# Kernel optimization log

Hardware: AMD Instinct MI355X
Metric: run time of the kernel (lower is better)

## Reference

```python
import jax, jax.numpy as jnp
import numpy as np

# OGB/PyG molecular featurization vocab sizes (x_map / e_map)
NODE_VOCABS = [119, 9, 11, 12, 10, 5, 8, 2, 2]   # 9 atom features
EDGE_VOCABS = [22, 6, 2]                          # 3 bond features
HID, OUT, LAYERS = 128, 256, 3
N_NODES, N_EDGES, N_GRAPHS = 200000, 400000, 8000
NODE_OFF = np.concatenate([[0], np.cumsum(NODE_VOCABS)[:-1]]).astype(np.int32)
EDGE_OFF = np.concatenate([[0], np.cumsum(EDGE_VOCABS)[:-1]]).astype(np.int32)
NODE_TOT = int(np.sum(NODE_VOCABS))
EDGE_TOT = int(np.sum(EDGE_VOCABS))


def setup_inputs() -> dict:
    key = jax.random.key(0)
    ks = jax.random.split(key, 16)
    # integer graph data (values in-range per categorical column via modulo)
    x = jax.random.randint(ks[0], (N_NODES, 9), 0, 1 << 30) % jnp.asarray(NODE_VOCABS)
    edge_attr = jax.random.randint(ks[1], (N_EDGES, 3), 0, 1 << 30) % jnp.asarray(EDGE_VOCABS)
    edge_index = jax.random.randint(ks[2], (2, N_EDGES), 0, N_NODES)
    batch = jnp.sort(jax.random.randint(ks[3], (N_NODES,), 0, N_GRAPHS))
    s = 0.02
    return {
        "x": x, "edge_attr": edge_attr, "edge_index": edge_index, "batch": batch,
        # embedding tables packed row-wise with per-feature offsets
        "node_emb": jax.random.normal(ks[4], (NODE_TOT, HID), jnp.float32) * s,
        "edge_emb": jax.random.normal(ks[5], (EDGE_TOT, HID), jnp.float32) * s,
        "node_proj_w": jax.random.normal(ks[6], (9 * HID, HID), jnp.float32) * s,
        "node_proj_b": jnp.zeros((HID,), jnp.float32),
        "edge_proj_w": jax.random.normal(ks[7], (3 * HID, HID), jnp.float32) * s,
        "edge_proj_b": jnp.zeros((HID,), jnp.float32),
        "mlp_w1": jax.random.normal(ks[8], (LAYERS, HID, HID), jnp.float32) * s,
        "mlp_b1": jnp.zeros((LAYERS, HID), jnp.float32),
        "mlp_w2": jax.random.normal(ks[9], (LAYERS, HID, HID), jnp.float32) * s,
        "mlp_b2": jnp.zeros((LAYERS, HID), jnp.float32),
        "proj_w": jax.random.normal(ks[10], (HID, OUT), jnp.float32) * s,
        "proj_b": jnp.zeros((OUT,), jnp.float32),
    }


def reference(x, edge_attr, edge_index, batch,
              node_emb, edge_emb,
              node_proj_w, node_proj_b, edge_proj_w, edge_proj_b,
              mlp_w1, mlp_b1, mlp_w2, mlp_b2, proj_w, proj_b):
    n = x.shape[0]
    e = edge_attr.shape[0]
    # embedding lookup per categorical column, concat, project -> [N, HID]
    nf = node_emb[x + jnp.asarray(NODE_OFF)].reshape(n, 9 * HID)
    h = nf @ node_proj_w + node_proj_b
    ef = edge_emb[edge_attr + jnp.asarray(EDGE_OFF)].reshape(e, 3 * HID)
    ef = ef @ edge_proj_w + edge_proj_b
    src, dst = edge_index[0], edge_index[1]
    for l in range(LAYERS):
        # GINEConv (eps=0): mlp(x + sum_{j->i} relu(x_j + e_ji)), then outer relu
        m = jax.nn.relu(h[src] + ef)                       # [E, HID] gather + fuse
        agg = jax.ops.segment_sum(m, dst, num_segments=N_NODES)
        z = h + agg
        z = jax.nn.relu(z @ mlp_w1[l] + mlp_b1[l]) @ mlp_w2[l] + mlp_b2[l]
        h = jax.nn.relu(z)
    g = jax.ops.segment_sum(h, batch, num_segments=N_GRAPHS)  # global_add_pool
    p = g @ proj_w + proj_b
    norm = jnp.maximum(jnp.linalg.norm(p, axis=-1, keepdims=True), 1e-12)
    return p / norm
```

## Files before the change

kernel.cpp:

```cpp
#include <hip/hip_runtime.h>
#include <hip/hip_bf16.h>

#define NN 200000
#define NE 400000
#define NG 8000
#define HID 128
#define OUTD 256
#define NODE_TOT 178
#define EDGE_TOT 30
#define NCOMBO 264
#define SCAN_NB 196

typedef __attribute__((ext_vector_type(8))) short bfrag8;
typedef __attribute__((ext_vector_type(4))) short bfrag4;
typedef __attribute__((ext_vector_type(4))) float f32x4;
typedef unsigned short ushort_t;

__constant__ int c_noff[10] = {0,119,128,139,151,161,166,174,176,178};

__device__ __forceinline__ ushort_t f2bf(float f) {
  union { float f; unsigned u; } x; x.f = f;
  unsigned r = x.u + 0x7fffu + ((x.u >> 16) & 1u);
  return (ushort_t)(r >> 16);
}
__device__ __forceinline__ float bf2f(ushort_t u) {
  union { unsigned u; float f; } x; x.u = ((unsigned)u) << 16;
  return x.f;
}

__global__ __launch_bounds__(128) void build_tables(
    const float* __restrict__ node_emb, const float* __restrict__ edge_emb,
    const float* __restrict__ npw, const float* __restrict__ npb,
    const float* __restrict__ epw, const float* __restrict__ epb,
    float* __restrict__ PN, float* __restrict__ PE)
{
  int r = blockIdx.x, d = threadIdx.x;
  if (r < NODE_TOT) {
    int c = 0;
    while (r >= c_noff[c+1]) c++;
    float acc = (c == 0) ? npb[d] : 0.f;
    const float* er = node_emb + r*HID;
    const float* wb = npw + (size_t)(c*HID)*HID + d;
    for (int k = 0; k < HID; k++) acc += er[k] * wb[(size_t)k*HID];
    PN[r*HID + d] = acc;
  } else {
    int re = r - NODE_TOT;
    int c = (re >= 28) ? 2 : (re >= 22 ? 1 : 0);
    float acc = (c == 0) ? epb[d] : 0.f;
    const float* er = edge_emb + re*HID;
    const float* wb = epw + (size_t)(c*HID)*HID + d;
    for (int k = 0; k < HID; k++) acc += er[k] * wb[(size_t)k*HID];
    PE[re*HID + d] = acc;
  }
}

__global__ __launch_bounds__(64) void build_pe3(const float* __restrict__ PE,
                                                unsigned* __restrict__ pe3b)
{
  int c = blockIdx.x, lane = threadIdx.x;
  int a2 = c & 1, a1 = (c >> 1) % 6, a0 = (c >> 1) / 6;
  int d = lane*2;
  float v0 = PE[a0*HID + d]   + PE[(22+a1)*HID + d]   + PE[(28+a2)*HID + d];
  float v1 = PE[a0*HID + d+1] + PE[(22+a1)*HID + d+1] + PE[(28+a2)*HID + d+1];
  pe3b[c*64 + lane] = (unsigned)f2bf(v0) | ((unsigned)f2bf(v1) << 16);
}

__global__ __launch_bounds__(256) void pack_w1(const float* __restrict__ w1,
                                               ushort_t* __restrict__ pw)
{
  int t = blockIdx.x*256 + threadIdx.x;
  int lane = t & 63, tile = (t >> 6) & 31, layer = t >> 11;
  int nt = tile >> 2, kt = tile & 3;
  int n  = nt*16 + (lane & 15);
  int k0 = kt*32 + ((lane >> 4) << 3);
  const float* src = w1 + (size_t)layer*HID*HID;
  ushort_t* dst = pw + (size_t)layer*32768 + (size_t)tile*512 + lane*8;
  #pragma unroll
  for (int j = 0; j < 8; j++) dst[j] = f2bf(src[(size_t)(k0+j)*HID + n]);
}

__global__ __launch_bounds__(256) void pack_w2(const float* __restrict__ w2,
                                               ushort_t* __restrict__ pw)
{
  int t = blockIdx.x*256 + threadIdx.x;
  int lane = t & 63, frag = (t >> 6) & 63, layer = t >> 12;
  int it = frag >> 3, kk = frag & 7;
  int i  = it*16 + (lane & 15);
  int k0 = kk*16 + ((lane >> 4) << 2);
  const float* src = w2 + (size_t)layer*HID*HID;
  ushort_t* dst = pw + (size_t)layer*32768 + 16384 + (size_t)frag*256 + lane*4;
  #pragma unroll
  for (int j = 0; j < 4; j++) dst[j] = f2bf(src[(size_t)(k0+j)*HID + i]);
}

__global__ __launch_bounds__(256) void node_embed(const int* __restrict__ x,
                                                  const float* __restrict__ PN,
                                                  ushort_t* __restrict__ h)
{
  int gid = blockIdx.x*256 + threadIdx.x;
  int i = gid >> 5, d0 = (gid & 31) << 2;
  const int* xr = x + i*9;
  f32x4 acc = {0.f, 0.f, 0.f, 0.f};
  #pragma unroll
  for (int c = 0; c < 9; c++)
    acc += *(const f32x4*)&PN[(c_noff[c] + xr[c])*HID + d0];
  uint2 pk;
  pk.x = (unsigned)f2bf(acc[0]) | ((unsigned)f2bf(acc[1]) << 16);
  pk.y = (unsigned)f2bf(acc[2]) | ((unsigned)f2bf(acc[3]) << 16);
  *(uint2*)&h[(size_t)i*HID + d0] = pk;
}

__global__ __launch_bounds__(256) void hist(const int* __restrict__ ei, int* __restrict__ deg) {
  int e = blockIdx.x*256 + threadIdx.x;
  if (e < NE) atomicAdd(&deg[ei[NE + e]], 1);
}

__global__ __launch_bounds__(256) void scan1(const int* __restrict__ deg,
                                             int* __restrict__ rowptr,
                                             int* __restrict__ bsum)
{
  __shared__ int sd[256];
  int b = blockIdx.x, t = threadIdx.x;
  int idx0 = b*1024 + t*4;
  int v[4]; int s = 0;
  #pragma unroll
  for (int j = 0; j < 4; j++) { int i = idx0 + j; v[j] = (i < NN) ? deg[i] : 0; s += v[j]; }
  sd[t] = s; __syncthreads();
  for (int off = 1; off < 256; off <<= 1) {
    int x = (t >= off) ? sd[t - off] : 0; __syncthreads();
    sd[t] += x; __syncthreads();
  }
  int run = (t > 0) ? sd[t-1] : 0;
  #pragma unroll
  for (int j = 0; j < 4; j++) { int i = idx0 + j; run += v[j]; if (i < NN) rowptr[i+1] = run; }
  if (t == 255) bsum[b] = sd[255];
}

__global__ __launch_bounds__(256) void scan2(int* __restrict__ bsum) {
  __shared__ int sd[256];
  int t = threadIdx.x;
  sd[t] = (t < SCAN_NB) ? bsum[t] : 0; __syncthreads();
  for (int off = 1; off < 256; off <<= 1) {
    int x = (t >= off) ? sd[t - off] : 0; __syncthreads();
    sd[t] += x; __syncthreads();
  }
  if (t < SCAN_NB) bsum[t] = sd[t];
}

__global__ __launch_bounds__(256) void scan3(int* __restrict__ rowptr, const int* __restrict__ bsum) {
  int b = blockIdx.x, t = threadIdx.x;
  if (b == 0) { if (t == 0) rowptr[0] = 0; return; }
  int add = bsum[b-1];
  int idx0 = b*1024 + t*4;
  #pragma unroll
  for (int j = 0; j < 4; j++) { int i = idx0 + j; if (i < NN) rowptr[i+1] += add; }
}

__global__ __launch_bounds__(256) void scatter_e(const int* __restrict__ ei,
                                                 const int* __restrict__ ea,
                                                 int* __restrict__ cursor,
                                                 unsigned* __restrict__ elist,
                                                 unsigned char* __restrict__ dloc)
{
  int e = blockIdx.x*256 + threadIdx.x;
  if (e >= NE) return;
  int src = ei[e], dst = ei[NE + e];
  const int* ar = ea + e*3;
  unsigned combo = (unsigned)((ar[0]*6 + ar[1])*2 + ar[2]);
  int pos = atomicAdd(&cursor[dst], 1);
  elist[pos] = (unsigned)src | (combo << 18);
  dloc[pos] = (unsigned char)(dst & 63);
}

template<bool LAST>
__global__ __launch_bounds__(256, 4) void gine_layer(
    const ushort_t* __restrict__ hin, ushort_t* __restrict__ hout,
    const int* __restrict__ rowptr, const unsigned* __restrict__ elist,
    const unsigned char* __restrict__ dloc,
    const unsigned* __restrict__ pe3b,
    const ushort_t* __restrict__ pw,
    const float* __restrict__ b1, const float* __restrict__ b2,
    const int* __restrict__ batch, float* __restrict__ gf)
{
  __shared__ ushort_t aggs[64*136];
  __shared__ int bids[64];
  int tid = threadIdx.x;
  int w = tid >> 6, lane = tid & 63;
  int q = lane >> 4;
  int rb = blockIdx.x*64 + w*16;
  const unsigned* h2 = (const unsigned*)hin;

  if (LAST && tid < 64) bids[tid] = batch[blockIdx.x*64 + tid];

  #pragma unroll
  for (int r = 0; r < 16; r++)
    ((unsigned*)&aggs[(w*16 + r)*136])[lane] = 0;

  int s = rowptr[rb], E = rowptr[rb + 16];
  int cur = -1;
  float ax = 0.f, ay = 0.f;

  auto proc = [&](int dl, unsigned hv, unsigned tt) {
    int dlu = __builtin_amdgcn_readfirstlane(dl);
    if (dlu != cur) {
      if (cur >= 0)
        ((unsigned*)&aggs[cur*136])[lane] =
            (unsigned)f2bf(ax) | ((unsigned)f2bf(ay) << 16);
      cur = dlu; ax = 0.f; ay = 0.f;
    }
    ax += fmaxf(bf2f((ushort_t)(hv & 0xffff)) + bf2f((ushort_t)(tt & 0xffff)), 0.f);
    ay += fmaxf(bf2f((ushort_t)(hv >> 16)) + bf2f((ushort_t)(tt >> 16)), 0.f);
  };

  int j = s;
  for (; j + 7 < E; j += 8) {
    unsigned pk[8]; int dl[8]; unsigned hv[8], tt[8];
    #pragma unroll
    for (int k = 0; k < 8; k++) { pk[k] = elist[j+k]; dl[k] = dloc[j+k]; }
    #pragma unroll
    for (int k = 0; k < 8; k++) {
      hv[k] = h2[(size_t)(pk[k] & 0x3ffff)*64 + lane];
      tt[k] = pe3b[(pk[k] >> 18)*64 + lane];
    }
    #pragma unroll
    for (int k = 0; k < 8; k++) proc(dl[k], hv[k], tt[k]);
  }
  for (; j < E; ++j) {
    unsigned pk = elist[j];
    int dl = dloc[j];
    unsigned hv = h2[(size_t)(pk & 0x3ffff)*64 + lane];
    unsigned tt = pe3b[(pk >> 18)*64 + lane];
    proc(dl, hv, tt);
  }
  if (cur >= 0)
    ((unsigned*)&aggs[cur*136])[lane] =
        (unsigned)f2bf(ax) | ((unsigned)f2bf(ay) << 16);

  int n = rb + (lane & 15);
  int acol = q << 3;

  bfrag8 afr[4];
  #pragma unroll
  for (int kt = 0; kt < 4; kt++) {
    int c = kt*32 + acol;
    bfrag8 hfr = *(const bfrag8*)(hin + (size_t)n*HID + c);
    bfrag8 gfr = *(const bfrag8*)&aggs[(w*16 + (lane & 15))*136 + c];
    bfrag8 fr;
    #pragma unroll
    for (int j2 = 0; j2 < 8; j2++)
      fr[j2] = (short)f2bf(bf2f((ushort_t)hfr[j2]) + bf2f((ushort_t)gfr[j2]));
    afr[kt] = fr;
  }

  if (LAST) __syncthreads();

  const bfrag8* w1f = (const bfrag8*)pw;
  const bfrag4* w2f = (const bfrag4*)(pw + 16384);

  f32x4 acc1[8];
  #pragma unroll
  for (int nt = 0; nt < 8; nt++)
    acc1[nt] = *(const f32x4*)&b1[nt*16 + q*4];
  #pragma unroll
  for (int kt = 0; kt < 4; kt++)
    #pragma unroll
    for (int nt = 0; nt < 8; nt++)
      acc1[nt] = __builtin_amdgcn_mfma_f32_16x16x32_bf16(w1f[(nt*4+kt)*64 + lane], afr[kt], acc1[nt], 0, 0, 0);

  bfrag4 t4[8];
  #pragma unroll
  for (int kk = 0; kk < 8; kk++) {
    bfrag4 v;
    #pragma unroll
    for (int r = 0; r < 4; r++) v[r] = (short)f2bf(fmaxf(acc1[kk][r], 0.f));
    t4[kk] = v;
  }

  #pragma unroll
  for (int it = 0; it < 8; it++) {
    f32x4 acc2 = *(const f32x4*)&b2[it*16 + q*4];
    #pragma unroll
    for (int kk = 0; kk < 8; kk++)
      acc2 = __builtin_amdgcn_mfma_f32_16x16x16bf16_1k(w2f[(it*8+kk)*64 + lane], t4[kk], acc2, 0, 0, 0);
    uint2 pk;
    pk.x = (unsigned)f2bf(fmaxf(acc2[0], 0.f)) | ((unsigned)f2bf(fmaxf(acc2[1], 0.f)) << 16);
    pk.y = (unsigned)f2bf(fmaxf(acc2[2], 0.f)) | ((unsigned)f2bf(fmaxf(acc2[3], 0.f)) << 16);
    if (LAST) {
      *(uint2*)&aggs[(w*16 + (lane & 15))*136 + it*16 + q*4] = pk;
    } else {
      *(uint2*)&hout[(size_t)n*HID + it*16 + q*4] = pk;
    }
  }

  if (LAST) {
    __syncthreads();
    int d = tid & 127, rh = tid >> 7;
    float acc = 0.f;
    int curg = bids[rh*32];
    for (int r = 0; r < 32; r++) {
      int row = rh*32 + r;
      int g = bids[row];
      if (g != curg) {
        atomicAdd(&gf[(size_t)curg*HID + d], acc);
        acc = 0.f; curg = g;
      }
      acc += bf2f(aggs[row*136 + d]);
    }
    atomicAdd(&gf[(size_t)curg*HID + d], acc);
  }
}

__global__ __launch_bounds__(256) void final_proj(const float* __restrict__ gf,
                                                  const float* __restrict__ W,
                                                  const float* __restrict__ b,
                                                  float* __restrict__ out)
{
  __shared__ float gls[16*128];
  __shared__ float part[16][4];
  int tid = threadIdx.x;
  int gbase = blockIdx.x*16;
  for (int idx = tid; idx < 2048; idx += 256) gls[idx] = gf[(size_t)gbase*128 + idx];
  __syncthreads();
  float acc[16];
  #pragma unroll
  for (int g = 0; g < 16; g++) acc[g] = 0.f;
  for (int k = 0; k < 128; k++) {
    float wv = W[(size_t)k*256 + tid];
    #pragma unroll
    for (int g = 0; g < 16; g++) acc[g] += gls[g*128 + k] * wv;
  }
  float bj = b[tid];
  int wid = tid >> 6, lane = tid & 63;
  #pragma unroll
  for (int g = 0; g < 16; g++) {
    acc[g] += bj;
    float s = acc[g]*acc[g];
    #pragma unroll
    for (int off = 32; off > 0; off >>= 1) s += __shfl_xor(s, off, 64);
    if (lane == 0) part[g][wid] = s;
  }
  __syncthreads();
  #pragma unroll
  for (int g = 0; g < 16; g++) {
    float S = part[g][0] + part[g][1] + part[g][2] + part[g][3];
    float rn = 1.f / fmaxf(sqrtf(S), 1e-12f);
    out[(size_t)(gbase + g)*256 + tid] = acc[g]*rn;
  }
}

__global__ __launch_bounds__(256) void ws_diag(float* __restrict__ out, int n, float wsval) {
  int i = blockIdx.x*256 + threadIdx.x;
  if (i < n) out[i] = (i == 0) ? wsval : 0.f;
}

extern "C" void kernel_launch(void* const* d_in, const int* in_sizes, int n_in,
                              void* d_out, int out_size, void* d_ws, size_t ws_size,
                              hipStream_t stream)
{
  const int*   x     = (const int*)d_in[0];
  const int*   ea    = (const int*)d_in[1];
  const int*   ei    = (const int*)d_in[2];
  const int*   batch = (const int*)d_in[3];
  const float* nemb  = (const float*)d_in[4];
  const float* eemb  = (const float*)d_in[5];
  const float* npw   = (const float*)d_in[6];
  const float* npb   = (const float*)d_in[7];
  const float* epw   = (const float*)d_in[8];
  const float* epb   = (const float*)d_in[9];
  const float* w1    = (const float*)d_in[10];
  const float* b1    = (const float*)d_in[11];
  const float* w2    = (const float*)d_in[12];
  const float* b2    = (const float*)d_in[13];
  const float* pjw   = (const float*)d_in[14];
  const float* pjb   = (const float*)d_in[15];
  float* out = (float*)d_out;

  char* ws = (char*)d_ws;
  size_t off = 0;
  auto carve = [&](size_t bytes) -> char* {
    char* p = ws + off;
    off = (off + bytes + 255) & ~(size_t)255;
    return p;
  };
  float*    PN     = (float*)carve((size_t)NODE_TOT*HID*4);
  float*    PE     = (float*)carve((size_t)EDGE_TOT*HID*4);
  unsigned* PE3b   = (unsigned*)carve((size_t)NCOMBO*64*4);
  ushort_t* PW     = (ushort_t*)carve((size_t)3*32768*2);
  ushort_t* hA     = (ushort_t*)carve((size_t)NN*HID*2);
  ushort_t* hB     = (ushort_t*)carve((size_t)NN*HID*2);
  float*    gf     = (float*)carve((size_t)NG*HID*4);
  int*      deg    = (int*)carve((size_t)NN*4);
  int*      rowptr = (int*)carve((size_t)(NN+1)*4);
  int*      cursor = (int*)carve((size_t)NN*4);
  int*      bsum   = (int*)carve((size_t)SCAN_NB*4);
  unsigned* elist  = (unsigned*)carve((size_t)NE*4);
  unsigned char* dlc = (unsigned char*)carve((size_t)NE);

  if (off > ws_size) {
    ws_diag<<<(out_size + 255)/256, 256, 0, stream>>>(out, out_size, (float)ws_size);
    return;
  }

  build_tables<<<NODE_TOT + EDGE_TOT, 128, 0, stream>>>(nemb, eemb, npw, npb, epw, epb, PN, PE);
  build_pe3<<<NCOMBO, 64, 0, stream>>>(PE, PE3b);
  pack_w1<<<24, 256, 0, stream>>>(w1, PW);
  pack_w2<<<48, 256, 0, stream>>>(w2, PW);
  node_embed<<<(NN*32)/256, 256, 0, stream>>>(x, PN, hA);

  hipMemsetAsync(deg, 0, (size_t)NN*4, stream);
  hipMemsetAsync(gf, 0, (size_t)NG*HID*4, stream);
  hist<<<(NE + 255)/256, 256, 0, stream>>>(ei, deg);
  scan1<<<SCAN_NB, 256, 0, stream>>>(deg, rowptr, bsum);
  scan2<<<1, 256, 0, stream>>>(bsum);
  scan3<<<SCAN_NB, 256, 0, stream>>>(rowptr, bsum);
  hipMemcpyAsync(cursor, rowptr, (size_t)NN*4, hipMemcpyDeviceToDevice, stream);
  scatter_e<<<(NE + 255)/256, 256, 0, stream>>>(ei, ea, cursor, elist, dlc);

  gine_layer<false><<<NN/64, 256, 0, stream>>>(hA, hB, rowptr, elist, dlc, PE3b,
                                               PW, b1, b2, batch, gf);
  gine_layer<false><<<NN/64, 256, 0, stream>>>(hB, hA, rowptr, elist, dlc, PE3b,
                                               PW + 32768, b1 + HID, b2 + HID, batch, gf);
  gine_layer<true><<<NN/64, 256, 0, stream>>>(hA, hB, rowptr, elist, dlc, PE3b,
                                              PW + 65536, b1 + 2*HID, b2 + 2*HID, batch, gf);

  final_proj<<<NG/16, 256, 0, stream>>>(gf, pjw, pjb, out);
}
```

Baseline: 447.9 us.

## Balance edge aggregation across warps with LDS float atomics and fuse setup launches

The edge aggregation in each GINE layer used to give every wavefront its own 16 destination rows, which left work unbalanced when degrees differed. It now splits the block's whole edge range evenly across the four wavefronts, and they accumulate into a shared fp32 LDS buffer with atomicAdd. Keeping the aggregate in fp32 also drops the bf16 rounding before the MLP. On the setup side, the two weight-pack kernels are merged, the scan writes the cursor copy directly so the memcpy goes away, and the two memsets become one. The cost is LDS atomic traffic, two atomics per element per edge, plus a larger shared-memory footprint that may lower occupancy.

```diff
diff --git a/kernel.cpp b/kernel.cpp
--- a/kernel.cpp
+++ b/kernel.cpp
@@ -10,6 +10,7 @@
 #define EDGE_TOT 30
 #define NCOMBO 264
 #define SCAN_NB 196
+#define AST 132
 
 typedef __attribute__((ext_vector_type(8))) short bfrag8;
 typedef __attribute__((ext_vector_type(4))) short bfrag4;
@@ -65,32 +66,31 @@
   pe3b[c*64 + lane] = (unsigned)f2bf(v0) | ((unsigned)f2bf(v1) << 16);
 }
 
-__global__ __launch_bounds__(256) void pack_w1(const float* __restrict__ w1,
-                                               ushort_t* __restrict__ pw)
+__global__ __launch_bounds__(256) void pack_w(const float* __restrict__ w1,
+                                              const float* __restrict__ w2,
+                                              ushort_t* __restrict__ pw)
 {
   int t = blockIdx.x*256 + threadIdx.x;
-  int lane = t & 63, tile = (t >> 6) & 31, layer = t >> 11;
-  int nt = tile >> 2, kt = tile & 3;
-  int n  = nt*16 + (lane & 15);
-  int k0 = kt*32 + ((lane >> 4) << 3);
-  const float* src = w1 + (size_t)layer*HID*HID;
-  ushort_t* dst = pw + (size_t)layer*32768 + (size_t)tile*512 + lane*8;
-  #pragma unroll
-  for (int j = 0; j < 8; j++) dst[j] = f2bf(src[(size_t)(k0+j)*HID + n]);
-}
-
-__global__ __launch_bounds__(256) void pack_w2(const float* __restrict__ w2,
-                                               ushort_t* __restrict__ pw)
-{
-  int t = blockIdx.x*256 + threadIdx.x;
-  int lane = t & 63, frag = (t >> 6) & 63, layer = t >> 12;
-  int it = frag >> 3, kk = frag & 7;
-  int i  = it*16 + (lane & 15);
-  int k0 = kk*16 + ((lane >> 4) << 2);
-  const float* src = w2 + (size_t)layer*HID*HID;
-  ushort_t* dst = pw + (size_t)layer*32768 + 16384 + (size_t)frag*256 + lane*4;
-  #pragma unroll
-  for (int j = 0; j < 4; j++) dst[j] = f2bf(src[(size_t)(k0+j)*HID + i]);
+  if (t < 6144) {
+    int lane = t & 63, tile = (t >> 6) & 31, layer = t >> 11;
+    int nt = tile >> 2, kt = tile & 3;
+    int n  = nt*16 + (lane & 15);
+    int k0 = kt*32 + ((lane >> 4) << 3);
+    const float* src = w1 + (size_t)layer*HID*HID;
+    ushort_t* dst = pw + (size_t)layer*32768 + (size_t)tile*512 + lane*8;
+    #pragma unroll
+    for (int j = 0; j < 8; j++) dst[j] = f2bf(src[(size_t)(k0+j)*HID + n]);
+  } else {
+    int t2 = t - 6144;
+    int lane = t2 & 63, frag = (t2 >> 6) & 63, layer = t2 >> 12;
+    int it = frag >> 3, kk = frag & 7;
+    int i  = it*16 + (lane & 15);
+    int k0 = kk*16 + ((lane >> 4) << 2);
+    const float* src = w2 + (size_t)layer*HID*HID;
+    ushort_t* dst = pw + (size_t)layer*32768 + 16384 + (size_t)frag*256 + lane*4;
+    #pragma unroll
+    for (int j = 0; j < 4; j++) dst[j] = f2bf(src[(size_t)(k0+j)*HID + i]);
+  }
 }
 
 __global__ __launch_bounds__(256) void node_embed(const int* __restrict__ x,
@@ -147,13 +147,23 @@
   if (t < SCAN_NB) bsum[t] = sd[t];
 }
 
-__global__ __launch_bounds__(256) void scan3(int* __restrict__ rowptr, const int* __restrict__ bsum) {
+__global__ __launch_bounds__(256) void scan3(int* __restrict__ rowptr,
+                                             const int* __restrict__ bsum,
+                                             int* __restrict__ cursor)
+{
   int b = blockIdx.x, t = threadIdx.x;
-  if (b == 0) { if (t == 0) rowptr[0] = 0; return; }
-  int add = bsum[b-1];
+  int add = (b > 0) ? bsum[b-1] : 0;
+  if (b == 0 && t == 0) { rowptr[0] = 0; cursor[0] = 0; }
   int idx0 = b*1024 + t*4;
   #pragma unroll
-  for (int j = 0; j < 4; j++) { int i = idx0 + j; if (i < NN) rowptr[i+1] += add; }
+  for (int j = 0; j < 4; j++) {
+    int i = idx0 + j;
+    if (i < NN) {
+      int v = rowptr[i+1] + add;
+      rowptr[i+1] = v;
+      cursor[i+1] = v;
+    }
+  }
 }
 
 __global__ __launch_bounds__(256) void scatter_e(const int* __restrict__ ei,
@@ -182,38 +192,27 @@
     const float* __restrict__ b1, const float* __restrict__ b2,
     const int* __restrict__ batch, float* __restrict__ gf)
 {
-  __shared__ ushort_t aggs[64*136];
+  __shared__ float aggs[64*AST];
   __shared__ int bids[64];
   int tid = threadIdx.x;
   int w = tid >> 6, lane = tid & 63;
   int q = lane >> 4;
-  int rb = blockIdx.x*64 + w*16;
+  int rb0 = blockIdx.x*64;
   const unsigned* h2 = (const unsigned*)hin;
 
-  if (LAST && tid < 64) bids[tid] = batch[blockIdx.x*64 + tid];
-
-  #pragma unroll
-  for (int r = 0; r < 16; r++)
-    ((unsigned*)&aggs[(w*16 + r)*136])[lane] = 0;
-
-  int s = rowptr[rb], E = rowptr[rb + 16];
-  int cur = -1;
-  float ax = 0.f, ay = 0.f;
-
-  auto proc = [&](int dl, unsigned hv, unsigned tt) {
-    int dlu = __builtin_amdgcn_readfirstlane(dl);
-    if (dlu != cur) {
-      if (cur >= 0)
-        ((unsigned*)&aggs[cur*136])[lane] =
-            (unsigned)f2bf(ax) | ((unsigned)f2bf(ay) << 16);
-      cur = dlu; ax = 0.f; ay = 0.f;
-    }
-    ax += fmaxf(bf2f((ushort_t)(hv & 0xffff)) + bf2f((ushort_t)(tt & 0xffff)), 0.f);
-    ay += fmaxf(bf2f((ushort_t)(hv >> 16)) + bf2f((ushort_t)(tt >> 16)), 0.f);
-  };
-
-  int j = s;
-  for (; j + 7 < E; j += 8) {
+  if (LAST && tid < 64) bids[tid] = batch[rb0 + tid];
+
+  for (int idx = tid; idx < 64*AST; idx += 256) aggs[idx] = 0.f;
+  __syncthreads();
+
+  int S = rowptr[rb0], E = rowptr[rb0 + 64];
+  int len = E - S;
+  int chunk = (len + 3) >> 2;
+  int cs = S + w*chunk;
+  int ce = min(cs + chunk, E);
+
+  int j = cs;
+  for (; j + 7 < ce; j += 8) {
     unsigned pk[8]; int dl[8]; unsigned hv[8], tt[8];
     #pragma unroll
     for (int k = 0; k < 8; k++) { pk[k] = elist[j+k]; dl[k] = dloc[j+k]; }
@@ -223,32 +222,43 @@
       tt[k] = pe3b[(pk[k] >> 18)*64 + lane];
     }
     #pragma unroll
-    for (int k = 0; k < 8; k++) proc(dl[k], hv[k], tt[k]);
-  }
-  for (; j < E; ++j) {
+    for (int k = 0; k < 8; k++) {
+      float vx = fmaxf(bf2f((ushort_t)(hv[k] & 0xffff)) + bf2f((ushort_t)(tt[k] & 0xffff)), 0.f);
+      float vy = fmaxf(bf2f((ushort_t)(hv[k] >> 16)) + bf2f((ushort_t)(tt[k] >> 16)), 0.f);
+      float* base = &aggs[dl[k]*AST + lane*2];
+      atomicAdd(base, vx);
+      atomicAdd(base + 1, vy);
+    }
+  }
+  for (; j < ce; ++j) {
     unsigned pk = elist[j];
     int dl = dloc[j];
     unsigned hv = h2[(size_t)(pk & 0x3ffff)*64 + lane];
     unsigned tt = pe3b[(pk >> 18)*64 + lane];
-    proc(dl, hv, tt);
-  }
-  if (cur >= 0)
-    ((unsigned*)&aggs[cur*136])[lane] =
-        (unsigned)f2bf(ax) | ((unsigned)f2bf(ay) << 16);
-
-  int n = rb + (lane & 15);
+    float vx = fmaxf(bf2f((ushort_t)(hv & 0xffff)) + bf2f((ushort_t)(tt & 0xffff)), 0.f);
+    float vy = fmaxf(bf2f((ushort_t)(hv >> 16)) + bf2f((ushort_t)(tt >> 16)), 0.f);
+    float* base = &aggs[dl*AST + lane*2];
+    atomicAdd(base, vx);
+    atomicAdd(base + 1, vy);
+  }
+  __syncthreads();
+
+  int n = rb0 + w*16 + (lane & 15);
   int acol = q << 3;
+  int arow = (w*16 + (lane & 15))*AST;
 
   bfrag8 afr[4];
   #pragma unroll
   for (int kt = 0; kt < 4; kt++) {
     int c = kt*32 + acol;
     bfrag8 hfr = *(const bfrag8*)(hin + (size_t)n*HID + c);
-    bfrag8 gfr = *(const bfrag8*)&aggs[(w*16 + (lane & 15))*136 + c];
+    f32x4 g0 = *(const f32x4*)&aggs[arow + c];
+    f32x4 g1 = *(const f32x4*)&aggs[arow + c + 4];
     bfrag8 fr;
     #pragma unroll
-    for (int j2 = 0; j2 < 8; j2++)
-      fr[j2] = (short)f2bf(bf2f((ushort_t)hfr[j2]) + bf2f((ushort_t)gfr[j2]));
+    for (int j2 = 0; j2 < 4; j2++) fr[j2]   = (short)f2bf(bf2f((ushort_t)hfr[j2])   + g0[j2]);
+    #pragma unroll
+    for (int j2 = 0; j2 < 4; j2++) fr[4+j2] = (short)f2bf(bf2f((ushort_t)hfr[4+j2]) + g1[j2]);
     afr[kt] = fr;
   }
 
@@ -282,12 +292,15 @@
     #pragma unroll
     for (int kk = 0; kk < 8; kk++)
       acc2 = __builtin_amdgcn_mfma_f32_16x16x16bf16_1k(w2f[(it*8+kk)*64 + lane], t4[kk], acc2, 0, 0, 0);
-    uint2 pk;
-    pk.x = (unsigned)f2bf(fmaxf(acc2[0], 0.f)) | ((unsigned)f2bf(fmaxf(acc2[1], 0.f)) << 16);
-    pk.y = (unsigned)f2bf(fmaxf(acc2[2], 0.f)) | ((unsigned)f2bf(fmaxf(acc2[3], 0.f)) << 16);
     if (LAST) {
-      *(uint2*)&aggs[(w*16 + (lane & 15))*136 + it*16 + q*4] = pk;
+      f32x4 rv;
+      #pragma unroll
+      for (int r = 0; r < 4; r++) rv[r] = fmaxf(acc2[r], 0.f);
+      *(f32x4*)&aggs[arow + it*16 + q*4] = rv;
     } else {
+      uint2 pk;
+      pk.x = (unsigned)f2bf(fmaxf(acc2[0], 0.f)) | ((unsigned)f2bf(fmaxf(acc2[1], 0.f)) << 16);
+      pk.y = (unsigned)f2bf(fmaxf(acc2[2], 0.f)) | ((unsigned)f2bf(fmaxf(acc2[3], 0.f)) << 16);
       *(uint2*)&hout[(size_t)n*HID + it*16 + q*4] = pk;
     }
   }
@@ -304,7 +317,7 @@
         atomicAdd(&gf[(size_t)curg*HID + d], acc);
         acc = 0.f; curg = g;
       }
-      acc += bf2f(aggs[row*136 + d]);
+      acc += aggs[row*AST + d];
     }
     atomicAdd(&gf[(size_t)curg*HID + d], acc);
   }
@@ -388,10 +401,10 @@
   ushort_t* PW     = (ushort_t*)carve((size_t)3*32768*2);
   ushort_t* hA     = (ushort_t*)carve((size_t)NN*HID*2);
   ushort_t* hB     = (ushort_t*)carve((size_t)NN*HID*2);
+  int*      deg    = (int*)carve((size_t)NN*4);
   float*    gf     = (float*)carve((size_t)NG*HID*4);
-  int*      deg    = (int*)carve((size_t)NN*4);
   int*      rowptr = (int*)carve((size_t)(NN+1)*4);
-  int*      cursor = (int*)carve((size_t)NN*4);
+  int*      cursor = (int*)carve((size_t)(NN+1)*4);
   int*      bsum   = (int*)carve((size_t)SCAN_NB*4);
   unsigned* elist  = (unsigned*)carve((size_t)NE*4);
   unsigned char* dlc = (unsigned char*)carve((size_t)NE);
@@ -403,17 +416,14 @@
 
   build_tables<<<NODE_TOT + EDGE_TOT, 128, 0, stream>>>(nemb, eemb, npw, npb, epw, epb, PN, PE);
   build_pe3<<<NCOMBO, 64, 0, stream>>>(PE, PE3b);
-  pack_w1<<<24, 256, 0, stream>>>(w1, PW);
-  pack_w2<<<48, 256, 0, stream>>>(w2, PW);
+  pack_w<<<72, 256, 0, stream>>>(w1, w2, PW);
   node_embed<<<(NN*32)/256, 256, 0, stream>>>(x, PN, hA);
 
-  hipMemsetAsync(deg, 0, (size_t)NN*4, stream);
-  hipMemsetAsync(gf, 0, (size_t)NG*HID*4, stream);
+  hipMemsetAsync(deg, 0, (size_t)NN*4 + (size_t)NG*HID*4, stream);
   hist<<<(NE + 255)/256, 256, 0, stream>>>(ei, deg);
   scan1<<<SCAN_NB, 256, 0, stream>>>(deg, rowptr, bsum);
   scan2<<<1, 256, 0, stream>>>(bsum);
-  scan3<<<SCAN_NB, 256, 0, stream>>>(rowptr, bsum);
-  hipMemcpyAsync(cursor, rowptr, (size_t)NN*4, hipMemcpyDeviceToDevice, stream);
+  scan3<<<SCAN_NB, 256, 0, stream>>>(rowptr, bsum, cursor);
   scatter_e<<<(NE + 255)/256, 256, 0, stream>>>(ei, ea, cursor, elist, dlc);
 
   gine_layer<false><<<NN/64, 256, 0, stream>>>(hA, hB, rowptr, elist, dlc, PE3b,
```

Result: slower. 1.090 ms (+143.4%).
